# Performance work log

Measured on AMD Instinct MI355X. Metric: run time of the kernel, lower is better.

## Reference

```python
import jax, jax.numpy as jnp
import numpy as np

IGNORE_INDEX = -100
BT, H, V = 2048, 4096, 32000


def setup_inputs() -> dict:
    key = jax.random.key(0)
    k1, k2, k3, k4 = jax.random.split(key, 4)
    _input = jax.random.normal(k1, (BT, H), dtype=jnp.float32) * 0.02
    lin_weight = jax.random.normal(k2, (V, H), dtype=jnp.float32) * 0.02
    bias = jnp.zeros((V,), dtype=jnp.float32)
    target = jax.random.randint(k3, (BT,), 0, V)
    loss_weights = jax.random.uniform(k4, (BT,), dtype=jnp.float32)
    reduce_sum_loss_weights = jnp.sum(loss_weights)  # scalar float32
    return {
        "lin_weight": lin_weight,
        "_input": _input,
        "target": target,
        "bias": bias,
        "loss_weights": loss_weights,
        "reduce_sum_loss_weights": reduce_sum_loss_weights,
        "grad_accumulation_steps": 1,
    }


def reference(lin_weight, _input, target, bias, loss_weights,
              reduce_sum_loss_weights, grad_accumulation_steps):
    # logits: (BT, V) -- the torch module chunks over BT to avoid materializing
    # this; as a correctness reference we compute it directly.
    logits = _input @ lin_weight.T + bias
    mask = target != IGNORE_INDEX                      # (BT,)
    n_non_ignore = jnp.maximum(mask.sum(), 1).astype(logits.dtype)
    safe_t = jnp.where(mask, target, 0)
    lse = jax.nn.logsumexp(logits, axis=-1)            # (BT,)
    gold = jnp.take_along_axis(logits, safe_t[:, None], axis=-1)[:, 0]
    # liger kernel with reduction='mean' divides per-row loss by n_non_ignore
    loss_1d = jnp.where(mask, (lse - gold) / n_non_ignore, 0.0)
    total = jnp.sum(loss_1d * loss_weights)
    rs = jnp.asarray(reduce_sum_loss_weights).reshape(())
    denom = jnp.where(rs == 0, 1.0, rs)
    loss = jnp.where(rs == 0, 0.0, total / denom)
    return loss / grad_accumulation_steps
```

## Files before the change

kernel.cpp:

```cpp
#include <hip/hip_runtime.h>
#include <hip/hip_bf16.h>
#include <math.h>

#define IGNORE_INDEX (-100)

constexpr int BT = 2048, H = 4096, V = 32000;
constexpr int BM = 256, BN = 256, BK = 64;
constexpr int KT = H / BK;
constexpr int MT2 = BT / BM;
constexpr int NT2 = V / BN;
constexpr int NCHUNK = NT2 * 4;

typedef __bf16 bf16x8 __attribute__((ext_vector_type(8)));
typedef float f32x4 __attribute__((ext_vector_type(4)));

__device__ __forceinline__ void gload_lds16(const __bf16* g, short* l) {
  __builtin_amdgcn_global_load_lds(
      (const __attribute__((address_space(1))) unsigned int*)(g),
      (__attribute__((address_space(3))) unsigned int*)(l), 16, 0, 0);
}

#define BAR()        asm volatile("s_barrier" ::: "memory")
#define WAIT_VM(N)   asm volatile("s_waitcnt vmcnt(" #N ")" ::: "memory")
#define SB0()        __builtin_amdgcn_sched_barrier(0)

__global__ __launch_bounds__(256)
void convert_bf16(const float* __restrict__ src, __bf16* __restrict__ dst,
                  int n8) {
  int i = blockIdx.x * blockDim.x + threadIdx.x;
  const int stride = gridDim.x * blockDim.x;
  for (; i < n8; i += stride) {
    const float4 f0 = ((const float4*)src)[2 * i];
    const float4 f1 = ((const float4*)src)[2 * i + 1];
    bf16x8 v;
    v[0] = (__bf16)f0.x; v[1] = (__bf16)f0.y;
    v[2] = (__bf16)f0.z; v[3] = (__bf16)f0.w;
    v[4] = (__bf16)f1.x; v[5] = (__bf16)f1.y;
    v[6] = (__bf16)f1.z; v[7] = (__bf16)f1.w;
    ((bf16x8*)dst)[i] = v;
  }
}

__global__ __launch_bounds__(512, 2)
void gemm_lse_8ph(const __bf16* __restrict__ Wb,
                  const __bf16* __restrict__ Xb,
                  const int* __restrict__ target,
                  const float* __restrict__ bias,
                  float* __restrict__ pM, float* __restrict__ pS,
                  float* __restrict__ gold)
{
  __shared__ short As[4 * 8192];
  __shared__ short Bs[4 * 8192];

  const int tid  = threadIdx.x;
  const int lane = tid & 63;
  const int wid  = tid >> 6;
  const int wr   = wid >> 2;
  const int wcol = wid & 3;

  const int bid = (int)blockIdx.x;
  const int swz = (bid & 7) * 125 + (bid >> 3);
  const int mt = swz & (MT2 - 1);
  const int nt = swz >> 3;
  const int m0 = mt * BM, n0 = nt * BN;

  const int l15 = lane & 15;
  const int j4  = lane >> 4;
  const int slotx = ((j4 ^ ((l15 >> 1) & 3)) & 3) << 3;
  const int abase = (wr * 128 + l15) * 32 + slotx;
  const int bbase = (wcol * 64 + l15) * 32 + slotx;

  const int srow = lane >> 2;
  const int sj8  = (((lane & 3) ^ ((lane >> 3) & 3)) << 3);

  const __bf16* ax0 = Xb + (size_t)(m0 + wid * 16 + srow) * H + sj8;
  const __bf16* ax1 = ax0 + (size_t)128 * H;
  const __bf16* bx0 = Wb + (size_t)(n0 + wid * 16 + srow) * H + sj8;
  const __bf16* bx1 = bx0 + (size_t)128 * H;

  f32x4 acc[8][4] = {};
  bf16x8 af[4], bfr[4];

#define STAGE_A(BUF, KH, DT)                                                  \
  { gload_lds16(ax0 + (DT) * BK + (KH) * 32,                                  \
                &As[(BUF) * 16384 + (KH) * 8192 + wid * 512]);                \
    gload_lds16(ax1 + (DT) * BK + (KH) * 32,                                  \
                &As[(BUF) * 16384 + (KH) * 8192 + (8 + wid) * 512]); }

#define STAGE_B(BUF, KH, DT)                                                  \
  { gload_lds16(bx0 + (DT) * BK + (KH) * 32,                                  \
                &Bs[(BUF) * 16384 + (KH) * 8192 + wid * 512]);                \
    gload_lds16(bx1 + (DT) * BK + (KH) * 32,                                  \
                &Bs[(BUF) * 16384 + (KH) * 8192 + (8 + wid) * 512]); }

#define READ_A(BUF, KH, MH)                                                   \
  { _Pragma("unroll")                                                         \
    for (int mi = 0; mi < 4; ++mi)                                            \
      af[mi] = *(const bf16x8*)&As[(BUF) * 16384 + (KH) * 8192 + abase +      \
                                   (MH) * 2048 + mi * 512]; }

#define READ_B(BUF, KH)                                                       \
  { _Pragma("unroll")                                                         \
    for (int ni = 0; ni < 4; ++ni)                                            \
      bfr[ni] = *(const bf16x8*)&Bs[(BUF) * 16384 + (KH) * 8192 + bbase +     \
                                    ni * 512]; }

#define MFMA16(MH)                                                            \
  { __builtin_amdgcn_s_setprio(1);                                            \
    _Pragma("unroll")                                                         \
    for (int mi = 0; mi < 4; ++mi)                                            \
      _Pragma("unroll")                                                       \
      for (int ni = 0; ni < 4; ++ni)                                          \
        acc[(MH) * 4 + mi][ni] = __builtin_amdgcn_mfma_f32_16x16x32_bf16(     \
            af[mi], bfr[ni], acc[(MH) * 4 + mi][ni], 0, 0, 0);                \
    __builtin_amdgcn_s_setprio(0); }

  STAGE_B(0, 0, 0); STAGE_A(0, 0, 0); STAGE_B(0, 1, 0); STAGE_A(0, 1, 0);
  STAGE_B(1, 0, 1); STAGE_A(1, 0, 1);
  WAIT_VM(4);
  BAR();

  for (int t = 0; t <= KT - 4; t += 2) {
    READ_A(0, 0, 0); READ_B(0, 0); STAGE_B(1, 1, 1);
    SB0(); BAR(); MFMA16(0);
    READ_A(0, 0, 1); STAGE_A(1, 1, 1);
    SB0(); BAR(); MFMA16(1);
    READ_A(0, 1, 0); READ_B(0, 1); STAGE_B(0, 0, 2);
    SB0(); BAR(); MFMA16(0);
    READ_A(0, 1, 1); STAGE_A(0, 0, 2);
    WAIT_VM(4); SB0(); BAR(); MFMA16(1);
    READ_A(1, 0, 0); READ_B(1, 0); STAGE_B(0, 1, 2);
    SB0(); BAR(); MFMA16(0);
    READ_A(1, 0, 1); STAGE_A(0, 1, 2);
    SB0(); BAR(); MFMA16(1);
    READ_A(1, 1, 0); READ_B(1, 1); STAGE_B(1, 0, 3);
    SB0(); BAR(); MFMA16(0);
    READ_A(1, 1, 1); STAGE_A(1, 0, 3);
    WAIT_VM(4); SB0(); BAR(); MFMA16(1);

    ax0 += 2 * BK; ax1 += 2 * BK; bx0 += 2 * BK; bx1 += 2 * BK;
  }

  READ_A(0, 0, 0); READ_B(0, 0); STAGE_B(1, 1, 1);
  SB0(); BAR(); MFMA16(0);
  READ_A(0, 0, 1); STAGE_A(1, 1, 1);
  SB0(); BAR(); MFMA16(1);
  READ_A(0, 1, 0); READ_B(0, 1);
  MFMA16(0);
  READ_A(0, 1, 1);
  WAIT_VM(0); SB0(); BAR(); MFMA16(1);
  READ_A(1, 0, 0); READ_B(1, 0);
  MFMA16(0);
  READ_A(1, 0, 1);
  MFMA16(1);
  READ_A(1, 1, 0); READ_B(1, 1);
  MFMA16(0);
  READ_A(1, 1, 1);
  MFMA16(1);

#undef STAGE_A
#undef STAGE_B
#undef READ_A
#undef READ_B
#undef MFMA16

  const int g = lane >> 4;
  const int c = lane & 15;
  const int colbase = n0 + wcol * 64;
  float bv[4];
#pragma unroll
  for (int ni = 0; ni < 4; ++ni) bv[ni] = bias[colbase + ni * 16 + c];

  const int chunk = nt * 4 + wcol;
#pragma unroll
  for (int mi = 0; mi < 8; ++mi) {
#pragma unroll
    for (int r = 0; r < 4; ++r) {
      const int row = m0 + wr * 128 + mi * 16 + g * 4 + r;
      const float v0 = acc[mi][0][r] + bv[0];
      const float v1 = acc[mi][1][r] + bv[1];
      const float v2 = acc[mi][2][r] + bv[2];
      const float v3 = acc[mi][3][r] + bv[3];
      float mx = fmaxf(fmaxf(v0, v1), fmaxf(v2, v3));
#pragma unroll
      for (int d = 1; d < 16; d <<= 1) mx = fmaxf(mx, __shfl_xor(mx, d));
      float s = expf(v0 - mx) + expf(v1 - mx) + expf(v2 - mx) + expf(v3 - mx);
#pragma unroll
      for (int d = 1; d < 16; d <<= 1) s += __shfl_xor(s, d);
      if (c == 0) {
        pM[(size_t)row * NCHUNK + chunk] = mx;
        pS[(size_t)row * NCHUNK + chunk] = s;
      }
      const int t = target[row];
      const int d0 = t - colbase;
      if (d0 >= 0 && d0 < 64 && c == (d0 & 15)) {
        const int nw = d0 >> 4;
        const float gv = (nw == 0) ? v0 : (nw == 1) ? v1 : (nw == 2) ? v2 : v3;
        gold[row] = gv;
      }
    }
  }
}

__global__ __launch_bounds__(256)
void reduce_lse(const float* __restrict__ pM, const float* __restrict__ pS,
                const float* __restrict__ gold, const int* __restrict__ target,
                const float* __restrict__ lw, float* __restrict__ rowterm)
{
  const int wid = threadIdx.x >> 6, lane = threadIdx.x & 63;
  const int row = blockIdx.x * 4 + wid;
  if (row >= BT) return;
  const float* pm = pM + (size_t)row * NCHUNK;
  const float* ps = pS + (size_t)row * NCHUNK;
  float m = -INFINITY;
  for (int c2 = lane; c2 < NCHUNK; c2 += 64) m = fmaxf(m, pm[c2]);
#pragma unroll
  for (int d = 1; d < 64; d <<= 1) m = fmaxf(m, __shfl_xor(m, d));
  float s = 0.f;
  for (int c2 = lane; c2 < NCHUNK; c2 += 64) s += ps[c2] * expf(pm[c2] - m);
#pragma unroll
  for (int d = 1; d < 64; d <<= 1) s += __shfl_xor(s, d);
  if (lane == 0) {
    const int t = target[row];
    float term = 0.f;
    if (t != IGNORE_INDEX) term = (m + logf(s) - gold[row]) * lw[row];
    rowterm[row] = term;
  }
}

__global__ __launch_bounds__(256)
void finalize(const float* __restrict__ rowterm, const int* __restrict__ target,
              const float* __restrict__ rsw, const int* __restrict__ gas,
              float* __restrict__ out)
{
  __shared__ float sred[4];
  __shared__ int cred[4];
  const int tid = threadIdx.x;
  float s = 0.f;
  int cnt = 0;
  for (int i = tid; i < BT; i += 256) {
    s += rowterm[i];
    cnt += (target[i] != IGNORE_INDEX) ? 1 : 0;
  }
#pragma unroll
  for (int d = 1; d < 64; d <<= 1) {
    s += __shfl_xor(s, d);
    cnt += __shfl_xor(cnt, d);
  }
  const int wid = tid >> 6, lane = tid & 63;
  if (lane == 0) { sred[wid] = s; cred[wid] = cnt; }
  __syncthreads();
  if (tid == 0) {
    const float st = sred[0] + sred[1] + sred[2] + sred[3];
    const int ct = cred[0] + cred[1] + cred[2] + cred[3];
    const float n = (float)((ct > 0) ? ct : 1);
    const float rs = rsw[0];
    float loss = (rs == 0.f) ? 0.f : (st / n) / rs;
    loss /= (float)gas[0];
    out[0] = loss;
  }
}

extern "C" void kernel_launch(void* const* d_in, const int* in_sizes, int n_in,
                              void* d_out, int out_size, void* d_ws, size_t ws_size,
                              hipStream_t stream)
{
  const float* Wt     = (const float*)d_in[0];
  const float* X      = (const float*)d_in[1];
  const int*   target = (const int*)d_in[2];
  const float* bias   = (const float*)d_in[3];
  const float* lw     = (const float*)d_in[4];
  const float* rsw    = (const float*)d_in[5];
  const int*   gas    = (const int*)d_in[6];
  float* out = (float*)d_out;

  const size_t nW = (size_t)V * H, nX = (size_t)BT * H;

  __bf16* Wb = (__bf16*)d_ws;
  __bf16* Xb = Wb + nW;
  float* pM = (float*)(Xb + nX);
  float* pS = pM + (size_t)BT * NCHUNK;
  float* gold = pS + (size_t)BT * NCHUNK;
  float* rowterm = gold + BT;

  convert_bf16<<<dim3(2048), dim3(256), 0, stream>>>(Wt, Wb, (int)(nW / 8));
  convert_bf16<<<dim3(256), dim3(256), 0, stream>>>(X, Xb, (int)(nX / 8));
  gemm_lse_8ph<<<dim3(MT2 * NT2), dim3(512), 0, stream>>>(Wb, Xb, target,
                                                          bias, pM, pS, gold);
  reduce_lse<<<dim3(BT / 4), dim3(256), 0, stream>>>(pM, pS, gold, target, lw,
                                                     rowterm);
  finalize<<<dim3(1), dim3(256), 0, stream>>>(rowterm, target, rsw, gas, out);
}
```

Measured before the change: 684.7 us.

## Double-buffer LDS fragment registers so reads overlap the previous MFMA phase

```diff
diff --git a/kernel.cpp b/kernel.cpp
--- a/kernel.cpp
+++ b/kernel.cpp
@@ -42,12 +42,12 @@
 }
 
 __global__ __launch_bounds__(512, 2)
-void gemm_lse_8ph(const __bf16* __restrict__ Wb,
-                  const __bf16* __restrict__ Xb,
-                  const int* __restrict__ target,
-                  const float* __restrict__ bias,
-                  float* __restrict__ pM, float* __restrict__ pS,
-                  float* __restrict__ gold)
+void gemm_lse_pipe(const __bf16* __restrict__ Wb,
+                   const __bf16* __restrict__ Xb,
+                   const int* __restrict__ target,
+                   const float* __restrict__ bias,
+                   float* __restrict__ pM, float* __restrict__ pS,
+                   float* __restrict__ gold)
 {
   __shared__ short As[4 * 8192];
   __shared__ short Bs[4 * 8192];
@@ -79,7 +79,7 @@
   const __bf16* bx1 = bx0 + (size_t)128 * H;
 
   f32x4 acc[8][4] = {};
-  bf16x8 af[4], bfr[4];
+  bf16x8 a0[4], a1[4], b0r[4], b1r[4];
 
 #define STAGE_A(BUF, KH, DT)                                                  \
   { gload_lds16(ax0 + (DT) * BK + (KH) * 32,                                  \
@@ -93,76 +93,90 @@
     gload_lds16(bx1 + (DT) * BK + (KH) * 32,                                  \
                 &Bs[(BUF) * 16384 + (KH) * 8192 + (8 + wid) * 512]); }
 
-#define READ_A(BUF, KH, MH)                                                   \
+#define RD_A(DST, BUF, KH, MH)                                                \
   { _Pragma("unroll")                                                         \
     for (int mi = 0; mi < 4; ++mi)                                            \
-      af[mi] = *(const bf16x8*)&As[(BUF) * 16384 + (KH) * 8192 + abase +      \
-                                   (MH) * 2048 + mi * 512]; }
-
-#define READ_B(BUF, KH)                                                       \
+      DST[mi] = *(const bf16x8*)&As[(BUF) * 16384 + (KH) * 8192 + abase +     \
+                                    (MH) * 2048 + mi * 512]; }
+
+#define RD_B(DST, BUF, KH)                                                    \
   { _Pragma("unroll")                                                         \
     for (int ni = 0; ni < 4; ++ni)                                            \
-      bfr[ni] = *(const bf16x8*)&Bs[(BUF) * 16384 + (KH) * 8192 + bbase +     \
+      DST[ni] = *(const bf16x8*)&Bs[(BUF) * 16384 + (KH) * 8192 + bbase +     \
                                     ni * 512]; }
 
-#define MFMA16(MH)                                                            \
+#define MF(ASET, BSET, MH)                                                    \
   { __builtin_amdgcn_s_setprio(1);                                            \
     _Pragma("unroll")                                                         \
     for (int mi = 0; mi < 4; ++mi)                                            \
       _Pragma("unroll")                                                       \
       for (int ni = 0; ni < 4; ++ni)                                          \
         acc[(MH) * 4 + mi][ni] = __builtin_amdgcn_mfma_f32_16x16x32_bf16(     \
-            af[mi], bfr[ni], acc[(MH) * 4 + mi][ni], 0, 0, 0);                \
+            ASET[mi], BSET[ni], acc[(MH) * 4 + mi][ni], 0, 0, 0);             \
     __builtin_amdgcn_s_setprio(0); }
 
   STAGE_B(0, 0, 0); STAGE_A(0, 0, 0); STAGE_B(0, 1, 0); STAGE_A(0, 1, 0);
   STAGE_B(1, 0, 1); STAGE_A(1, 0, 1);
   WAIT_VM(4);
-  BAR();
+  RD_A(a0, 0, 0, 0); RD_B(b0r, 0, 0);
+  SB0(); BAR();
 
   for (int t = 0; t <= KT - 4; t += 2) {
-    READ_A(0, 0, 0); READ_B(0, 0); STAGE_B(1, 1, 1);
-    SB0(); BAR(); MFMA16(0);
-    READ_A(0, 0, 1); STAGE_A(1, 1, 1);
-    SB0(); BAR(); MFMA16(1);
-    READ_A(0, 1, 0); READ_B(0, 1); STAGE_B(0, 0, 2);
-    SB0(); BAR(); MFMA16(0);
-    READ_A(0, 1, 1); STAGE_A(0, 0, 2);
-    WAIT_VM(4); SB0(); BAR(); MFMA16(1);
-    READ_A(1, 0, 0); READ_B(1, 0); STAGE_B(0, 1, 2);
-    SB0(); BAR(); MFMA16(0);
-    READ_A(1, 0, 1); STAGE_A(0, 1, 2);
-    SB0(); BAR(); MFMA16(1);
-    READ_A(1, 1, 0); READ_B(1, 1); STAGE_B(1, 0, 3);
-    SB0(); BAR(); MFMA16(0);
-    READ_A(1, 1, 1); STAGE_A(1, 0, 3);
-    WAIT_VM(4); SB0(); BAR(); MFMA16(1);
+    STAGE_B(1, 1, 1);
+    RD_A(a1, 0, 0, 1);
+    SB0(); BAR(); MF(a0, b0r, 0);
+    STAGE_A(1, 1, 1);
+    RD_A(a0, 0, 1, 0); RD_B(b1r, 0, 1);
+    SB0(); BAR(); MF(a1, b0r, 1);
+    STAGE_B(0, 0, 2);
+    RD_A(a1, 0, 1, 1);
+    SB0(); BAR(); MF(a0, b1r, 0);
+    STAGE_A(0, 0, 2);
+    WAIT_VM(4);
+    RD_A(a0, 1, 0, 0); RD_B(b0r, 1, 0);
+    SB0(); BAR(); MF(a1, b1r, 1);
+    STAGE_B(0, 1, 2);
+    RD_A(a1, 1, 0, 1);
+    SB0(); BAR(); MF(a0, b0r, 0);
+    STAGE_A(0, 1, 2);
+    RD_A(a0, 1, 1, 0); RD_B(b1r, 1, 1);
+    SB0(); BAR(); MF(a1, b0r, 1);
+    STAGE_B(1, 0, 3);
+    RD_A(a1, 1, 1, 1);
+    SB0(); BAR(); MF(a0, b1r, 0);
+    STAGE_A(1, 0, 3);
+    WAIT_VM(4);
+    RD_A(a0, 0, 0, 0); RD_B(b0r, 0, 0);
+    SB0(); BAR(); MF(a1, b1r, 1);
 
     ax0 += 2 * BK; ax1 += 2 * BK; bx0 += 2 * BK; bx1 += 2 * BK;
   }
 
-  READ_A(0, 0, 0); READ_B(0, 0); STAGE_B(1, 1, 1);
-  SB0(); BAR(); MFMA16(0);
-  READ_A(0, 0, 1); STAGE_A(1, 1, 1);
-  SB0(); BAR(); MFMA16(1);
-  READ_A(0, 1, 0); READ_B(0, 1);
-  MFMA16(0);
-  READ_A(0, 1, 1);
-  WAIT_VM(0); SB0(); BAR(); MFMA16(1);
-  READ_A(1, 0, 0); READ_B(1, 0);
-  MFMA16(0);
-  READ_A(1, 0, 1);
-  MFMA16(1);
-  READ_A(1, 1, 0); READ_B(1, 1);
-  MFMA16(0);
-  READ_A(1, 1, 1);
-  MFMA16(1);
+  STAGE_B(1, 1, 1);
+  RD_A(a1, 0, 0, 1);
+  SB0(); BAR(); MF(a0, b0r, 0);
+  STAGE_A(1, 1, 1);
+  RD_A(a0, 0, 1, 0); RD_B(b1r, 0, 1);
+  SB0(); BAR(); MF(a1, b0r, 1);
+  RD_A(a1, 0, 1, 1);
+  SB0(); BAR(); MF(a0, b1r, 0);
+  WAIT_VM(4);
+  RD_A(a0, 1, 0, 0); RD_B(b0r, 1, 0);
+  SB0(); BAR(); MF(a1, b1r, 1);
+  RD_A(a1, 1, 0, 1);
+  SB0(); BAR(); MF(a0, b0r, 0);
+  WAIT_VM(0);
+  RD_A(a0, 1, 1, 0); RD_B(b1r, 1, 1);
+  SB0(); BAR(); MF(a1, b0r, 1);
+  RD_A(a1, 1, 1, 1);
+  SB0(); BAR(); MF(a0, b1r, 0);
+  MF(a1, b1r, 1);
 
 #undef STAGE_A
 #undef STAGE_B
-#undef READ_A
-#undef READ_B
-#undef MFMA16
+#undef RD_A
+#undef RD_B
+#undef MF
 
   const int g = lane >> 4;
   const int c = lane & 15;
@@ -285,8 +299,8 @@
 
   convert_bf16<<<dim3(2048), dim3(256), 0, stream>>>(Wt, Wb, (int)(nW / 8));
   convert_bf16<<<dim3(256), dim3(256), 0, stream>>>(X, Xb, (int)(nX / 8));
-  gemm_lse_8ph<<<dim3(MT2 * NT2), dim3(512), 0, stream>>>(Wb, Xb, target,
-                                                          bias, pM, pS, gold);
+  gemm_lse_pipe<<<dim3(MT2 * NT2), dim3(512), 0, stream>>>(Wb, Xb, target,
+                                                           bias, pM, pS, gold);
   reduce_lse<<<dim3(BT / 4), dim3(256), 0, stream>>>(pM, pS, gold, target, lw,
                                                      rowterm);
   finalize<<<dim3(1), dim3(256), 0, stream>>>(rowterm, target, rsw, gas, out);
```

New measurement: 676.1 us. No clear change (-1.2%).
